# Kernel tuning notes

Hardware: AMD Instinct MI355X
Metric: run time of the kernel (lower is better)

The kernel has to match this reference:

```python
import jax, jax.numpy as jnp
import numpy as np

N_DETS = 50000
DEG = 32
N_EDGES = N_DETS * DEG

def _xavier(key, fan_in, fan_out):
    lim = np.sqrt(6.0 / (fan_in + fan_out)).astype(np.float32)
    return jax.random.uniform(key, (fan_in, fan_out), jnp.float32, -lim, lim)

def setup_inputs() -> dict:
    key = jax.random.key(0)
    ks = jax.random.split(key, 10)
    detFeatures = jax.random.normal(ks[0], (N_DETS, 128), jnp.float32)
    # every detection has exactly DEG neighbor pairs -> sorted segment ids, no empty segments
    cIdxs = jnp.repeat(jnp.arange(N_DETS, dtype=jnp.int64), DEG)
    nIdxs = jax.random.randint(ks[1], (N_EDGES,), 0, N_DETS, jnp.int64)
    pairFeatures = jax.random.normal(ks[2], (N_EDGES, 32), jnp.float32)
    return {
        "detFeatures": detFeatures,
        "cIdxs": cIdxs,
        "nIdxs": nIdxs,
        "pairFeatures": pairFeatures,
        "W_fc1": _xavier(ks[3], 128, 32), "b_fc1": jnp.zeros((32,), jnp.float32),
        "W_pw1": _xavier(ks[4], 96, 64), "b_pw1": jnp.zeros((64,), jnp.float32),
        "W_pw2": _xavier(ks[5], 64, 64), "b_pw2": jnp.zeros((64,), jnp.float32),
        "W_pm1": _xavier(ks[6], 64, 64), "b_pm1": jnp.zeros((64,), jnp.float32),
        "W_pm2": _xavier(ks[7], 64, 64), "b_pm2": jnp.zeros((64,), jnp.float32),
        "W_out": _xavier(ks[8], 64, 128), "b_out": jnp.zeros((128,), jnp.float32),
    }

def reference(detFeatures, cIdxs, nIdxs, pairFeatures,
              W_fc1, b_fc1, W_pw1, b_pw1, W_pw2, b_pw2,
              W_pm1, b_pm1, W_pm2, b_pm2, W_out, b_out):
    relu = jax.nn.relu
    # fc1: [N,128] -> [N,32]
    h = relu(detFeatures @ W_fc1 + b_fc1)
    # gather center / neighbor feats per pair; zero neighbor feats on identity rows
    cFeats = h[cIdxs]                                   # [E,32]
    nFeats = jnp.where((cIdxs == nIdxs)[:, None], 0.0, h[nIdxs])  # [E,32]
    x = jnp.concatenate((pairFeatures, cFeats, nFeats), axis=1)   # [E,96]
    x = relu(x @ W_pw1 + b_pw1)                         # [E,64]
    x = relu(x @ W_pw2 + b_pw2)                         # [E,64]
    # per-detection segment max (replaces the O(N) python loop)
    m = jax.ops.segment_max(x, cIdxs, num_segments=detFeatures.shape[0])  # [N,64]
    m = relu(m @ W_pm1 + b_pm1)
    m = relu(m @ W_pm2 + b_pm2)
    refined = m @ W_out + b_out                         # [N,128]
    return relu(detFeatures + refined)
```

## Files before the change

kernel.cpp:

```cpp
#include <hip/hip_runtime.h>

#define NDET 50000
#define DEG 32
#define NEDGE (NDET * DEG)
#define NGROUP (NEDGE / 64)

typedef __attribute__((ext_vector_type(8))) short short8;
typedef __attribute__((ext_vector_type(4))) float f32x4;

__device__ inline unsigned short f2bf(float x) {
    return (unsigned short)((__builtin_bit_cast(unsigned int, x) + 0x8000u) >> 16);
}

__device__ inline short8 pack8(f32x4 a, f32x4 b) {
    short8 r;
    r[0] = (short)f2bf(a[0]); r[1] = (short)f2bf(a[1]);
    r[2] = (short)f2bf(a[2]); r[3] = (short)f2bf(a[3]);
    r[4] = (short)f2bf(b[0]); r[5] = (short)f2bf(b[1]);
    r[6] = (short)f2bf(b[2]); r[7] = (short)f2bf(b[3]);
    return r;
}

__global__ __launch_bounds__(256, 4) void fc1_kernel(
    const float* __restrict__ detF,
    const float* __restrict__ W,
    const float* __restrict__ b,
    unsigned short* __restrict__ hbf)
{
    __shared__ __align__(16) unsigned short WT[32 * 136];

    const int tid  = threadIdx.x;
    const int lane = tid & 63;
    const int wv   = tid >> 6;
    const int m16  = lane & 15;
    const int q    = lane >> 4;

    for (int i = tid; i < 32 * 128; i += 256) {
        int n = i >> 7, k = i & 127;
        WT[n * 136 + k] = f2bf(W[k * 32 + n]);
    }
    __syncthreads();

    const int t = blockIdx.x * 4 + wv;
    if (t >= NDET / 16) return;
    const int r0 = t * 16;

    f32x4 acc[2];
#pragma unroll
    for (int nt = 0; nt < 2; nt++) {
        float c0 = b[nt * 16 + m16];
        acc[nt] = (f32x4){c0, c0, c0, c0};
    }

#pragma unroll
    for (int ks = 0; ks < 4; ks++) {
        const float* pr = detF + (size_t)(r0 + m16) * 128 + ks * 32 + q * 8;
        short8 a = pack8(*(const f32x4*)pr, *(const f32x4*)(pr + 4));
#pragma unroll
        for (int nt = 0; nt < 2; nt++) {
            short8 bf = *(const short8*)&WT[(nt * 16 + m16) * 136 + ks * 32 + q * 8];
            acc[nt] = __builtin_amdgcn_mfma_f32_16x16x32_bf16(a, bf, acc[nt], 0, 0, 0);
        }
    }

#pragma unroll
    for (int r = 0; r < 4; r++) {
        int row = r0 + q * 4 + r;
#pragma unroll
        for (int nt = 0; nt < 2; nt++)
            hbf[(size_t)row * 32 + nt * 16 + m16] = f2bf(fmaxf(acc[nt][r], 0.0f));
    }
}

__global__ __launch_bounds__(256, 4) void edge_kernel(
    const unsigned short* __restrict__ hbf,
    const int* __restrict__ nIdx,
    const float* __restrict__ pairF,
    const float* __restrict__ W1,
    const float* __restrict__ b1,
    const float* __restrict__ W2,
    const float* __restrict__ b2,
    unsigned short* __restrict__ m_bf)
{
    __shared__ __align__(16) unsigned short W1T[64 * 104];
    __shared__ __align__(16) unsigned short W2T[64 * 72];
    __shared__ __align__(16) unsigned short Y1s[4][32 * 72];

    const int tid  = threadIdx.x;
    const int lane = tid & 63;
    const int wv   = tid >> 6;
    const int m16  = lane & 15;
    const int q    = lane >> 4;

    for (int i = tid; i < 64 * 96; i += 256) {
        int n = i / 96, k = i - n * 96;
        W1T[n * 104 + k] = f2bf(W1[k * 64 + n]);
    }
    for (int i = tid; i < 64 * 64; i += 256) {
        int n = i >> 6, k = i & 63;
        W2T[n * 72 + k] = f2bf(W2[k * 64 + n]);
    }
    __syncthreads();

    float b1r[4], b2r[4];
#pragma unroll
    for (int nt = 0; nt < 4; nt++) {
        b1r[nt] = b1[nt * 16 + m16];
        b2r[nt] = b2[nt * 16 + m16];
    }

    unsigned short* Y1w = &Y1s[wv][0];

    const int wstride = (int)gridDim.x * 4;
    int g = blockIdx.x * 4 + wv;
    if (g >= NGROUP) return;

    const short8 zr = {0, 0, 0, 0, 0, 0, 0, 0};

    int    ni[4];
    int    sk[4];
    short8 nb[4];
    f32x4  pv[4][2];

#pragma unroll
    for (int mt = 0; mt < 4; mt++)
        ni[mt] = __builtin_nontemporal_load(&nIdx[g * 64 + mt * 16 + m16]);
#pragma unroll
    for (int mt = 0; mt < 4; mt++) {
        const float* pr = pairF + (size_t)(g * 64 + mt * 16 + m16) * 32 + q * 8;
        pv[mt][0] = __builtin_nontemporal_load((const f32x4*)pr);
        pv[mt][1] = __builtin_nontemporal_load((const f32x4*)(pr + 4));
    }
#pragma unroll
    for (int mt = 0; mt < 4; mt++) {
        sk[mt] = (ni[mt] == g * 2 + (mt >> 1));
        nb[mt] = *(const short8*)&hbf[(size_t)ni[mt] * 32 + q * 8];
    }
    {
        int g1 = g + wstride;
        int gl = (g1 < NGROUP) ? g1 : g;
#pragma unroll
        for (int mt = 0; mt < 4; mt++)
            ni[mt] = __builtin_nontemporal_load(&nIdx[gl * 64 + mt * 16 + m16]);
    }

    while (true) {
        const int d0 = g * 2;
        const int gn = g + wstride;
        const bool more = (gn < NGROUP);
        const int gt  = more ? gn : g;
        const int gnn = gn + wstride;
        const int gl2 = (more && gnn < NGROUP) ? gnn : gt;

        short8 ap[4];
#pragma unroll
        for (int mt = 0; mt < 4; mt++) ap[mt] = pack8(pv[mt][0], pv[mt][1]);
#pragma unroll
        for (int mt = 0; mt < 4; mt++) {
            const float* pr = pairF + (size_t)(gt * 64 + mt * 16 + m16) * 32 + q * 8;
            pv[mt][0] = __builtin_nontemporal_load((const f32x4*)pr);
            pv[mt][1] = __builtin_nontemporal_load((const f32x4*)(pr + 4));
        }

#pragma unroll
        for (int mt = 0; mt < 4; mt++)
            if (sk[mt]) nb[mt] = zr;
        short8 ac2[2];
        ac2[0] = *(const short8*)&hbf[(size_t)d0 * 32 + q * 8];
        ac2[1] = *(const short8*)&hbf[(size_t)(d0 + 1) * 32 + q * 8];

#pragma unroll
        for (int h = 0; h < 2; h++) {
            f32x4 acc[2][4];

#pragma unroll
            for (int j = 0; j < 2; j++)
#pragma unroll
                for (int nt = 0; nt < 4; nt++) {
                    float c0 = b1r[nt];
                    acc[j][nt] = (f32x4){c0, c0, c0, c0};
                }
#pragma unroll
            for (int nt = 0; nt < 4; nt++) {
                const unsigned short* wb = &W1T[(nt * 16 + m16) * 104 + q * 8];
                short8 w0 = *(const short8*)&wb[0];
                acc[0][nt] = __builtin_amdgcn_mfma_f32_16x16x32_bf16(ap[2 * h],     w0, acc[0][nt], 0, 0, 0);
                acc[1][nt] = __builtin_amdgcn_mfma_f32_16x16x32_bf16(ap[2 * h + 1], w0, acc[1][nt], 0, 0, 0);
                short8 w1 = *(const short8*)&wb[64];
                acc[0][nt] = __builtin_amdgcn_mfma_f32_16x16x32_bf16(nb[2 * h],     w1, acc[0][nt], 0, 0, 0);
                acc[1][nt] = __builtin_amdgcn_mfma_f32_16x16x32_bf16(nb[2 * h + 1], w1, acc[1][nt], 0, 0, 0);
                short8 w2 = *(const short8*)&wb[32];
                acc[0][nt] = __builtin_amdgcn_mfma_f32_16x16x32_bf16(ac2[h], w2, acc[0][nt], 0, 0, 0);
                acc[1][nt] = __builtin_amdgcn_mfma_f32_16x16x32_bf16(ac2[h], w2, acc[1][nt], 0, 0, 0);
            }

            {
                const int m0 = 2 * h, m1 = 2 * h + 1;
                nb[m0] = *(const short8*)&hbf[(size_t)ni[m0] * 32 + q * 8];
                sk[m0] = (ni[m0] == gt * 2 + h);
                nb[m1] = *(const short8*)&hbf[(size_t)ni[m1] * 32 + q * 8];
                sk[m1] = (ni[m1] == gt * 2 + h);
                ni[m0] = __builtin_nontemporal_load(&nIdx[gl2 * 64 + m0 * 16 + m16]);
                ni[m1] = __builtin_nontemporal_load(&nIdx[gl2 * 64 + m1 * 16 + m16]);
            }

#pragma unroll
            for (int j = 0; j < 2; j++)
#pragma unroll
                for (int nt = 0; nt < 4; nt++)
#pragma unroll
                    for (int r = 0; r < 4; r++)
                        Y1w[(j * 16 + q * 4 + r) * 72 + nt * 16 + m16] =
                            f2bf(fmaxf(acc[j][nt][r], 0.0f));

            short8 af0[2], af1[2];
#pragma unroll
            for (int j = 0; j < 2; j++) {
                af0[j] = *(const short8*)&Y1w[(j * 16 + m16) * 72 + q * 8];
                af1[j] = *(const short8*)&Y1w[(j * 16 + m16) * 72 + 32 + q * 8];
            }
#pragma unroll
            for (int j = 0; j < 2; j++)
#pragma unroll
                for (int nt = 0; nt < 4; nt++) {
                    float c0 = b2r[nt];
                    acc[j][nt] = (f32x4){c0, c0, c0, c0};
                }
#pragma unroll
            for (int nt = 0; nt < 4; nt++) {
                short8 wf = *(const short8*)&W2T[(nt * 16 + m16) * 72 + q * 8];
                acc[0][nt] = __builtin_amdgcn_mfma_f32_16x16x32_bf16(af0[0], wf, acc[0][nt], 0, 0, 0);
                acc[1][nt] = __builtin_amdgcn_mfma_f32_16x16x32_bf16(af0[1], wf, acc[1][nt], 0, 0, 0);
                wf = *(const short8*)&W2T[(nt * 16 + m16) * 72 + 32 + q * 8];
                acc[0][nt] = __builtin_amdgcn_mfma_f32_16x16x32_bf16(af1[0], wf, acc[0][nt], 0, 0, 0);
                acc[1][nt] = __builtin_amdgcn_mfma_f32_16x16x32_bf16(af1[1], wf, acc[1][nt], 0, 0, 0);
            }

#pragma unroll
            for (int nt = 0; nt < 4; nt++) {
                float v = 0.0f;
#pragma unroll
                for (int j = 0; j < 2; j++)
#pragma unroll
                    for (int r = 0; r < 4; r++) v = fmaxf(v, acc[j][nt][r]);
                v = fmaxf(v, __shfl_xor(v, 16));
                v = fmaxf(v, __shfl_xor(v, 32));
                if (q == 0) m_bf[(size_t)(d0 + h) * 64 + nt * 16 + m16] = f2bf(v);
            }
        }

        if (!more) break;
        g = gn;
    }
}

__global__ __launch_bounds__(256, 2) void tail_kernel(
    const float* __restrict__ detF,
    const unsigned short* __restrict__ m_bf,
    const float* __restrict__ Wm1, const float* __restrict__ bm1,
    const float* __restrict__ Wm2, const float* __restrict__ bm2,
    const float* __restrict__ Wo,  const float* __restrict__ bo,
    float* __restrict__ out)
{
    __shared__ __align__(16) unsigned short W1T[64 * 72];
    __shared__ __align__(16) unsigned short W2T[64 * 72];
    __shared__ __align__(16) unsigned short WoT[128 * 72];
    __shared__ __align__(16) unsigned short Tt[4][64 * 72];

    const int tid  = threadIdx.x;
    const int lane = tid & 63;
    const int wv   = tid >> 6;
    const int m16  = lane & 15;
    const int q    = lane >> 4;

    for (int i = tid; i < 64 * 64; i += 256) {
        int n = i >> 6, k = i & 63;
        W1T[n * 72 + k] = f2bf(Wm1[k * 64 + n]);
        W2T[n * 72 + k] = f2bf(Wm2[k * 64 + n]);
    }
    for (int i = tid; i < 128 * 64; i += 256) {
        int n = i >> 6, k = i & 63;
        WoT[n * 72 + k] = f2bf(Wo[k * 128 + n]);
    }
    __syncthreads();

    float bm1r[4], bm2r[4], bor[8];
#pragma unroll
    for (int nt = 0; nt < 4; nt++) {
        bm1r[nt] = bm1[nt * 16 + m16];
        bm2r[nt] = bm2[nt * 16 + m16];
    }
#pragma unroll
    for (int nt = 0; nt < 8; nt++) bor[nt] = bo[nt * 16 + m16];

    unsigned short* Tw = &Tt[wv][0];
    const int NTG = (NDET + 63) / 64;

    for (int gI = blockIdx.x * 4 + wv; gI < NTG; gI += (int)gridDim.x * 4) {
        const int d0 = gI * 64;

        f32x4 acc[4][4];
#pragma unroll
        for (int mt = 0; mt < 4; mt++)
#pragma unroll
            for (int nt = 0; nt < 4; nt++) {
                float c0 = bm1r[nt];
                acc[mt][nt] = (f32x4){c0, c0, c0, c0};
            }
#pragma unroll
        for (int ks = 0; ks < 2; ks++) {
            short8 af[4];
#pragma unroll
            for (int mt = 0; mt < 4; mt++) {
                int row = d0 + mt * 16 + m16;
                if (row >= NDET) row = NDET - 1;
                af[mt] = *(const short8*)&m_bf[(size_t)row * 64 + ks * 32 + q * 8];
            }
#pragma unroll
            for (int mt = 0; mt < 4; mt++)
#pragma unroll
                for (int nt = 0; nt < 4; nt++) {
                    short8 bf = *(const short8*)&W1T[(nt * 16 + m16) * 72 + ks * 32 + q * 8];
                    acc[mt][nt] = __builtin_amdgcn_mfma_f32_16x16x32_bf16(af[mt], bf, acc[mt][nt], 0, 0, 0);
                }
        }
#pragma unroll
        for (int mt = 0; mt < 4; mt++)
#pragma unroll
            for (int nt = 0; nt < 4; nt++)
#pragma unroll
                for (int r = 0; r < 4; r++)
                    Tw[(mt * 16 + q * 4 + r) * 72 + nt * 16 + m16] =
                        f2bf(fmaxf(acc[mt][nt][r], 0.0f));

#pragma unroll
        for (int mt = 0; mt < 4; mt++)
#pragma unroll
            for (int nt = 0; nt < 4; nt++) {
                float c0 = bm2r[nt];
                acc[mt][nt] = (f32x4){c0, c0, c0, c0};
            }
#pragma unroll
        for (int ks = 0; ks < 2; ks++) {
            short8 af[4];
#pragma unroll
            for (int mt = 0; mt < 4; mt++)
                af[mt] = *(const short8*)&Tw[(mt * 16 + m16) * 72 + ks * 32 + q * 8];
#pragma unroll
            for (int mt = 0; mt < 4; mt++)
#pragma unroll
                for (int nt = 0; nt < 4; nt++) {
                    short8 bf = *(const short8*)&W2T[(nt * 16 + m16) * 72 + ks * 32 + q * 8];
                    acc[mt][nt] = __builtin_amdgcn_mfma_f32_16x16x32_bf16(af[mt], bf, acc[mt][nt], 0, 0, 0);
                }
        }
#pragma unroll
        for (int mt = 0; mt < 4; mt++)
#pragma unroll
            for (int nt = 0; nt < 4; nt++)
#pragma unroll
                for (int r = 0; r < 4; r++)
                    Tw[(mt * 16 + q * 4 + r) * 72 + nt * 16 + m16] =
                        f2bf(fmaxf(acc[mt][nt][r], 0.0f));

        short8 a3[4][2];
#pragma unroll
        for (int ks = 0; ks < 2; ks++)
#pragma unroll
            for (int mt = 0; mt < 4; mt++)
                a3[mt][ks] = *(const short8*)&Tw[(mt * 16 + m16) * 72 + ks * 32 + q * 8];

#pragma unroll
        for (int h2 = 0; h2 < 2; h2++) {
            f32x4 acc3[4][4];
#pragma unroll
            for (int mt = 0; mt < 4; mt++)
#pragma unroll
                for (int nt = 0; nt < 4; nt++) {
                    float c0 = bor[h2 * 4 + nt];
                    acc3[mt][nt] = (f32x4){c0, c0, c0, c0};
                }
#pragma unroll
            for (int ks = 0; ks < 2; ks++)
#pragma unroll
                for (int mt = 0; mt < 4; mt++)
#pragma unroll
                    for (int nt = 0; nt < 4; nt++) {
                        short8 bf = *(const short8*)&WoT[((h2 * 4 + nt) * 16 + m16) * 72 + ks * 32 + q * 8];
                        acc3[mt][nt] = __builtin_amdgcn_mfma_f32_16x16x32_bf16(a3[mt][ks], bf, acc3[mt][nt], 0, 0, 0);
                    }
#pragma unroll
            for (int mt = 0; mt < 4; mt++)
#pragma unroll
                for (int r = 0; r < 4; r++) {
                    int row = d0 + mt * 16 + q * 4 + r;
                    if (row < NDET) {
#pragma unroll
                        for (int nt = 0; nt < 4; nt++) {
                            int col = (h2 * 4 + nt) * 16 + m16;
                            float v = detF[(size_t)row * 128 + col] + acc3[mt][nt][r];
                            out[(size_t)row * 128 + col] = fmaxf(v, 0.0f);
                        }
                    }
                }
        }
    }
}

extern "C" void kernel_launch(void* const* d_in, const int* in_sizes, int n_in,
                              void* d_out, int out_size, void* d_ws, size_t ws_size,
                              hipStream_t stream)
{
    const float* detF  = (const float*)d_in[0];
    const int*   nIdx  = (const int*)d_in[2];
    const float* pairF = (const float*)d_in[3];
    const float* W_fc1 = (const float*)d_in[4];
    const float* b_fc1 = (const float*)d_in[5];
    const float* W_pw1 = (const float*)d_in[6];
    const float* b_pw1 = (const float*)d_in[7];
    const float* W_pw2 = (const float*)d_in[8];
    const float* b_pw2 = (const float*)d_in[9];
    const float* W_pm1 = (const float*)d_in[10];
    const float* b_pm1 = (const float*)d_in[11];
    const float* W_pm2 = (const float*)d_in[12];
    const float* b_pm2 = (const float*)d_in[13];
    const float* W_out = (const float*)d_in[14];
    const float* b_out = (const float*)d_in[15];
    float* out = (float*)d_out;

    unsigned short* hbf  = (unsigned short*)d_ws;
    unsigned short* m_bf = hbf + (size_t)NDET * 32;

    fc1_kernel<<<(NDET / 16 + 3) / 4, 256, 0, stream>>>(detF, W_fc1, b_fc1, hbf);
    edge_kernel<<<1024, 256, 0, stream>>>(hbf, nIdx, pairF,
                                          W_pw1, b_pw1, W_pw2, b_pw2, m_bf);
    tail_kernel<<<256, 256, 0, stream>>>(detF, m_bf, W_pm1, b_pm1, W_pm2, b_pm2,
                                         W_out, b_out, out);
}
```

Measured before the change: 499.5 us.

## Restructure edge-kernel prefetch pipeline and raise wave priority around MFMA blocks

Stops double-buffering pairFeatures across iterations: the current group's pair features are now loaded at the top of each iteration, which frees the pv registers held over the loop. The neighbor-row gathers and next-next index loads are hoisted ahead of both MFMA halves instead of being interleaved after each half. The identity-row zeroing goes into a separate register copy. s_setprio brackets the MFMA sections so waves doing matrix math get issue priority. This trades lower register pressure and earlier gather issue for exposing the pairFeatures load latency inside each iteration.

```diff
diff --git a/kernel.cpp b/kernel.cpp
--- a/kernel.cpp
+++ b/kernel.cpp
@@ -120,17 +120,10 @@
     int    ni[4];
     int    sk[4];
     short8 nb[4];
-    f32x4  pv[4][2];
 
 #pragma unroll
     for (int mt = 0; mt < 4; mt++)
         ni[mt] = __builtin_nontemporal_load(&nIdx[g * 64 + mt * 16 + m16]);
-#pragma unroll
-    for (int mt = 0; mt < 4; mt++) {
-        const float* pr = pairF + (size_t)(g * 64 + mt * 16 + m16) * 32 + q * 8;
-        pv[mt][0] = __builtin_nontemporal_load((const f32x4*)pr);
-        pv[mt][1] = __builtin_nontemporal_load((const f32x4*)(pr + 4));
-    }
 #pragma unroll
     for (int mt = 0; mt < 4; mt++) {
         sk[mt] = (ni[mt] == g * 2 + (mt >> 1));
@@ -148,27 +141,40 @@
         const int d0 = g * 2;
         const int gn = g + wstride;
         const bool more = (gn < NGROUP);
-        const int gt  = more ? gn : g;
-        const int gnn = gn + wstride;
-        const int gl2 = (more && gnn < NGROUP) ? gnn : gt;
-
-        short8 ap[4];
-#pragma unroll
-        for (int mt = 0; mt < 4; mt++) ap[mt] = pack8(pv[mt][0], pv[mt][1]);
+        const int gt = more ? gn : g;
+
+        f32x4 pv[4][2];
 #pragma unroll
         for (int mt = 0; mt < 4; mt++) {
-            const float* pr = pairF + (size_t)(gt * 64 + mt * 16 + m16) * 32 + q * 8;
+            const float* pr = pairF + (size_t)(g * 64 + mt * 16 + m16) * 32 + q * 8;
             pv[mt][0] = __builtin_nontemporal_load((const f32x4*)pr);
             pv[mt][1] = __builtin_nontemporal_load((const f32x4*)(pr + 4));
         }
-
-#pragma unroll
-        for (int mt = 0; mt < 4; mt++)
-            if (sk[mt]) nb[mt] = zr;
         short8 ac2[2];
         ac2[0] = *(const short8*)&hbf[(size_t)d0 * 32 + q * 8];
         ac2[1] = *(const short8*)&hbf[(size_t)(d0 + 1) * 32 + q * 8];
 
+        short8 ap[4], an[4];
+#pragma unroll
+        for (int mt = 0; mt < 4; mt++) {
+            ap[mt] = pack8(pv[mt][0], pv[mt][1]);
+            an[mt] = sk[mt] ? zr : nb[mt];
+        }
+
+#pragma unroll
+        for (int mt = 0; mt < 4; mt++) {
+            int s = (ni[mt] == gt * 2 + (mt >> 1));
+            nb[mt] = *(const short8*)&hbf[(size_t)ni[mt] * 32 + q * 8];
+            sk[mt] = s;
+        }
+        {
+            const int gnn = gn + wstride;
+            const int gl2 = (more && gnn < NGROUP) ? gnn : gt;
+#pragma unroll
+            for (int mt = 0; mt < 4; mt++)
+                ni[mt] = __builtin_nontemporal_load(&nIdx[gl2 * 64 + mt * 16 + m16]);
+        }
+
 #pragma unroll
         for (int h = 0; h < 2; h++) {
             f32x4 acc[2][4];
@@ -180,6 +186,7 @@
                     float c0 = b1r[nt];
                     acc[j][nt] = (f32x4){c0, c0, c0, c0};
                 }
+            __builtin_amdgcn_s_setprio(1);
 #pragma unroll
             for (int nt = 0; nt < 4; nt++) {
                 const unsigned short* wb = &W1T[(nt * 16 + m16) * 104 + q * 8];
@@ -187,22 +194,13 @@
                 acc[0][nt] = __builtin_amdgcn_mfma_f32_16x16x32_bf16(ap[2 * h],     w0, acc[0][nt], 0, 0, 0);
                 acc[1][nt] = __builtin_amdgcn_mfma_f32_16x16x32_bf16(ap[2 * h + 1], w0, acc[1][nt], 0, 0, 0);
                 short8 w1 = *(const short8*)&wb[64];
-                acc[0][nt] = __builtin_amdgcn_mfma_f32_16x16x32_bf16(nb[2 * h],     w1, acc[0][nt], 0, 0, 0);
-                acc[1][nt] = __builtin_amdgcn_mfma_f32_16x16x32_bf16(nb[2 * h + 1], w1, acc[1][nt], 0, 0, 0);
+                acc[0][nt] = __builtin_amdgcn_mfma_f32_16x16x32_bf16(an[2 * h],     w1, acc[0][nt], 0, 0, 0);
+                acc[1][nt] = __builtin_amdgcn_mfma_f32_16x16x32_bf16(an[2 * h + 1], w1, acc[1][nt], 0, 0, 0);
                 short8 w2 = *(const short8*)&wb[32];
                 acc[0][nt] = __builtin_amdgcn_mfma_f32_16x16x32_bf16(ac2[h], w2, acc[0][nt], 0, 0, 0);
                 acc[1][nt] = __builtin_amdgcn_mfma_f32_16x16x32_bf16(ac2[h], w2, acc[1][nt], 0, 0, 0);
             }
-
-            {
-                const int m0 = 2 * h, m1 = 2 * h + 1;
-                nb[m0] = *(const short8*)&hbf[(size_t)ni[m0] * 32 + q * 8];
-                sk[m0] = (ni[m0] == gt * 2 + h);
-                nb[m1] = *(const short8*)&hbf[(size_t)ni[m1] * 32 + q * 8];
-                sk[m1] = (ni[m1] == gt * 2 + h);
-                ni[m0] = __builtin_nontemporal_load(&nIdx[gl2 * 64 + m0 * 16 + m16]);
-                ni[m1] = __builtin_nontemporal_load(&nIdx[gl2 * 64 + m1 * 16 + m16]);
-            }
+            __builtin_amdgcn_s_setprio(0);
 
 #pragma unroll
             for (int j = 0; j < 2; j++)
@@ -226,6 +224,7 @@
                     float c0 = b2r[nt];
                     acc[j][nt] = (f32x4){c0, c0, c0, c0};
                 }
+            __builtin_amdgcn_s_setprio(1);
 #pragma unroll
             for (int nt = 0; nt < 4; nt++) {
                 short8 wf = *(const short8*)&W2T[(nt * 16 + m16) * 72 + q * 8];
@@ -235,6 +234,7 @@
                 acc[0][nt] = __builtin_amdgcn_mfma_f32_16x16x32_bf16(af1[0], wf, acc[0][nt], 0, 0, 0);
                 acc[1][nt] = __builtin_amdgcn_mfma_f32_16x16x32_bf16(af1[1], wf, acc[1][nt], 0, 0, 0);
             }
+            __builtin_amdgcn_s_setprio(0);
 
 #pragma unroll
             for (int nt = 0; nt < 4; nt++) {
```

New measurement: 449.5 us. 1.11x faster.
